# Kernel tuning notes

Measured on AMD Instinct MI355X. Metric: run time of the kernel, lower is better.

## Reference

```python
import jax, jax.numpy as jnp
import numpy as np


def setup_inputs() -> dict:
    key = jax.random.key(0)
    ks = jax.random.split(key, 6)
    B = 65536
    x = jax.random.normal(ks[0], (B, 784), dtype=jnp.float32)
    conv_w = jax.random.normal(ks[1], (3, 3), dtype=jnp.float32)
    fc1_w = jax.random.normal(ks[2], (100, 676), dtype=jnp.float32) * (1.0 / np.sqrt(676))
    fc1_b = jax.random.normal(ks[3], (100,), dtype=jnp.float32) * 0.01
    fc2_w = jax.random.normal(ks[4], (10, 100), dtype=jnp.float32) * (1.0 / np.sqrt(100))
    fc2_b = jax.random.normal(ks[5], (10,), dtype=jnp.float32) * 0.01
    return {"x": x, "conv_w": conv_w, "fc1_w": fc1_w, "fc1_b": fc1_b, "fc2_w": fc2_w, "fc2_b": fc2_b}


def reference(x, conv_w, fc1_w, fc1_b, fc2_w, fc2_b):
    B = x.shape[0]
    img = x.reshape(B, 1, 28, 28)  # NCHW, single channel
    kern = conv_w.reshape(1, 1, 3, 3)  # OIHW
    # 'valid' cross-correlation, matching the slicing-based Convolve()
    conv = jax.lax.conv_general_dilated(
        img, kern, window_strides=(1, 1), padding='VALID',
        dimension_numbers=('NCHW', 'OIHW', 'NCHW'))  # [B,1,26,26]
    h = conv.reshape(B, 26 * 26)
    h = jax.nn.relu(h @ fc1_w.T + fc1_b)
    out = h @ fc2_w.T + fc2_b
    return out
```

## Files before the change

### kernel.cpp

```cpp
#include <hip/hip_runtime.h>


typedef short  s16x8 __attribute__((ext_vector_type(8)));
typedef float  f32x4 __attribute__((ext_vector_type(4)));

#define BM   16
#define CSTR 712
#define HSTR 132
#define NT   8
#define KC   22

__device__ __forceinline__ unsigned short f2bf(float f) {
    unsigned int u = __builtin_bit_cast(unsigned int, f);
    u = (u + 0x7fffu + ((u >> 16) & 1u)) >> 16;
    return (unsigned short)u;
}

extern "C" __global__ void __launch_bounds__(256)
prep_w1(const float* __restrict__ W1, const float* __restrict__ b1,
        unsigned short* __restrict__ bw)
{
    int id = blockIdx.x * 256 + threadIdx.x;
    if (id >= NT * KC * 64) return;
    int lane = id & 63;
    int kc   = (id >> 6) % KC;
    int t    = id / (KC * 64);
    int n    = t * 16 + (lane & 15);
    int k0   = kc * 32 + (lane >> 4) * 8;
    unsigned short v[8];
#pragma unroll
    for (int j = 0; j < 8; ++j) {
        int k = k0 + j;
        float f = 0.f;
        if (n < 100) {
            if (k < 676)       f = W1[(size_t)n * 676 + k];
            else if (k == 676) f = b1[n];
        }
        v[j] = f2bf(f);
    }
    *(uint4*)(bw + (size_t)id * 8) = *(const uint4*)v;
}

extern "C" __global__ void __launch_bounds__(256, 6)
digit_model_fused(const float* __restrict__ x,
                  const float* __restrict__ cw9,
                  const unsigned short* __restrict__ bw,
                  const float* __restrict__ W2,
                  const float* __restrict__ b2,
                  float* __restrict__ out)
{
    __shared__ __align__(16) unsigned char smem[BM * CSTR * 2];
    unsigned short* cbuf = (unsigned short*)smem;
    float*          hbuf = (float*)smem;

    const int tid  = threadIdx.x;
    const int lane = tid & 63;
    const int wv   = tid >> 6;
    const int q    = lane >> 4;
    const int mn   = lane & 15;
    const int m0   = blockIdx.x * BM;

    float cw[9];
#pragma unroll
    for (int i = 0; i < 9; ++i) cw[i] = cw9[i];

    for (int p = tid; p < BM * 18; p += 256) {
        int mi = p / 18, qq = p - mi * 18;
        *(unsigned int*)(cbuf + mi * CSTR + 676 + qq * 2) = (qq == 0) ? 0x3F80u : 0u;
    }

    for (int task = tid; task < BM * 52; task += 256) {
        int mi = task / 52, rh = task - mi * 52, r = rh >> 1, h = rh & 1;
        const float* ip = x + (size_t)(m0 + mi) * 784 + r * 28 + h * 12;
        float acc[13];
#pragma unroll
        for (int c = 0; c < 13; ++c) acc[c] = 0.f;
#pragma unroll
        for (int dr = 0; dr < 3; ++dr) {
            float rowv[16];
            const float4* rp = (const float4*)(ip + dr * 28);
#pragma unroll
            for (int g = 0; g < 4; ++g) {
                float4 v = rp[g];
                rowv[g*4+0] = v.x; rowv[g*4+1] = v.y;
                rowv[g*4+2] = v.z; rowv[g*4+3] = v.w;
            }
#pragma unroll
            for (int dc = 0; dc < 3; ++dc) {
                float w = cw[dr*3+dc];
#pragma unroll
                for (int c = 0; c < 13; ++c)
                    acc[c] = fmaf(rowv[c + dc + h], w, acc[c]);
            }
        }
        unsigned short* dst = cbuf + mi * CSTR + r * 26 + h * 13;
        if (h == 0) {
#pragma unroll
            for (int c = 0; c < 12; c += 2)
                *(unsigned int*)(dst + c) =
                    (unsigned int)f2bf(acc[c]) | ((unsigned int)f2bf(acc[c+1]) << 16);
            dst[12] = f2bf(acc[12]);
        } else {
            dst[0] = f2bf(acc[0]);
#pragma unroll
            for (int c = 1; c < 13; c += 2)
                *(unsigned int*)(dst + c) =
                    (unsigned int)f2bf(acc[c]) | ((unsigned int)f2bf(acc[c+1]) << 16);
        }
    }
    __syncthreads();

    f32x4 acc0, acc1;
#pragma unroll
    for (int i = 0; i < 4; ++i) { acc0[i] = 0.f; acc1[i] = 0.f; }

    const unsigned short* arow = cbuf + mn * CSTR + q * 8;
    const uint4* bwv = (const uint4*)bw;
    const int t0 = wv, t1 = wv + 4;

    uint4 a  = *(const uint4*)(arow);
    uint4 b0 = bwv[(t0 * KC) * 64 + lane];
    uint4 b1 = bwv[(t1 * KC) * 64 + lane];
    for (int kc = 0; kc < KC; ++kc) {
        int kn = (kc + 1 < KC) ? kc + 1 : kc;
        uint4 na  = *(const uint4*)(arow + kn * 32);
        uint4 nb0 = bwv[(t0 * KC + kn) * 64 + lane];
        uint4 nb1 = bwv[(t1 * KC + kn) * 64 + lane];
        acc0 = __builtin_amdgcn_mfma_f32_16x16x32_bf16(
                   __builtin_bit_cast(s16x8, a), __builtin_bit_cast(s16x8, b0),
                   acc0, 0, 0, 0);
        acc1 = __builtin_amdgcn_mfma_f32_16x16x32_bf16(
                   __builtin_bit_cast(s16x8, a), __builtin_bit_cast(s16x8, b1),
                   acc1, 0, 0, 0);
        a = na; b0 = nb0; b1 = nb1;
    }
    __syncthreads();

#pragma unroll
    for (int r = 0; r < 4; ++r) {
        int row = q * 4 + r;
        float v0 = acc0[r]; v0 = v0 > 0.f ? v0 : 0.f;
        float v1 = acc1[r]; v1 = v1 > 0.f ? v1 : 0.f;
        hbuf[row * HSTR + t0 * 16 + mn] = v0;
        hbuf[row * HSTR + t1 * 16 + mn] = v1;
    }
    __syncthreads();

    for (int p = tid; p < BM * 10; p += 256) {
        int mi = p / 10, o = p - mi * 10;
        const float4* hv = (const float4*)(hbuf + mi * HSTR);
        const float4* w2 = (const float4*)(W2 + (size_t)o * 100);
        float s = b2[o];
#pragma unroll
        for (int g = 0; g < 25; ++g) {
            float4 h4 = hv[g], w4 = w2[g];
            s += h4.x*w4.x + h4.y*w4.y + h4.z*w4.z + h4.w*w4.w;
        }
        out[(size_t)(m0 + mi) * 10 + o] = s;
    }
}

extern "C" void kernel_launch(void* const* d_in, const int* in_sizes, int n_in,
                              void* d_out, int out_size, void* d_ws, size_t ws_size,
                              hipStream_t stream) {
    const float* x  = (const float*)d_in[0];
    const float* cw = (const float*)d_in[1];
    const float* W1 = (const float*)d_in[2];
    const float* b1 = (const float*)d_in[3];
    const float* W2 = (const float*)d_in[4];
    const float* b2 = (const float*)d_in[5];
    float* out = (float*)d_out;
    unsigned short* bw = (unsigned short*)d_ws;

    const int B = in_sizes[0] / 784;

    hipLaunchKernelGGL(prep_w1, dim3((NT * KC * 64 + 255) / 256), dim3(256),
                       0, stream, W1, b1, bw);
    hipLaunchKernelGGL(digit_model_fused, dim3(B / BM), dim3(256), 0, stream,
                       x, cw, bw, W2, b2, out);
}
```

Baseline: 327.8 us.

## Double row tile to 32 and reuse each W1 fragment across two MFMA row blocks

Raises the rows per block from 16 to 32 so each loaded W1 fragment feeds two MFMA row tiles. This halves the global W1 traffic per output row. The conv stage now gives each thread a full 26-wide output row instead of half a row, cutting redundant input loads. In exchange, LDS per block doubles, the occupancy hint drops from 6 to 4, register pressure rises, and the grid has half as many blocks.

```diff
diff --git a/kernel.cpp b/kernel.cpp
--- a/kernel.cpp
+++ b/kernel.cpp
@@ -4,7 +4,7 @@
 typedef short  s16x8 __attribute__((ext_vector_type(8)));
 typedef float  f32x4 __attribute__((ext_vector_type(4)));
 
-#define BM   16
+#define BM   32
 #define CSTR 712
 #define HSTR 132
 #define NT   8
@@ -41,7 +41,7 @@
     *(uint4*)(bw + (size_t)id * 8) = *(const uint4*)v;
 }
 
-extern "C" __global__ void __launch_bounds__(256, 6)
+extern "C" __global__ void __launch_bounds__(256, 4)
 digit_model_fused(const float* __restrict__ x,
                   const float* __restrict__ cw9,
                   const unsigned short* __restrict__ bw,
@@ -69,18 +69,18 @@
         *(unsigned int*)(cbuf + mi * CSTR + 676 + qq * 2) = (qq == 0) ? 0x3F80u : 0u;
     }
 
-    for (int task = tid; task < BM * 52; task += 256) {
-        int mi = task / 52, rh = task - mi * 52, r = rh >> 1, h = rh & 1;
-        const float* ip = x + (size_t)(m0 + mi) * 784 + r * 28 + h * 12;
-        float acc[13];
+    for (int task = tid; task < BM * 26; task += 256) {
+        int mi = task / 26, r = task - mi * 26;
+        const float* ip = x + (size_t)(m0 + mi) * 784 + r * 28;
+        float acc[26];
 #pragma unroll
-        for (int c = 0; c < 13; ++c) acc[c] = 0.f;
+        for (int c = 0; c < 26; ++c) acc[c] = 0.f;
 #pragma unroll
         for (int dr = 0; dr < 3; ++dr) {
-            float rowv[16];
+            float rowv[28];
             const float4* rp = (const float4*)(ip + dr * 28);
 #pragma unroll
-            for (int g = 0; g < 4; ++g) {
+            for (int g = 0; g < 7; ++g) {
                 float4 v = rp[g];
                 rowv[g*4+0] = v.x; rowv[g*4+1] = v.y;
                 rowv[g*4+2] = v.z; rowv[g*4+3] = v.w;
@@ -89,60 +89,55 @@
             for (int dc = 0; dc < 3; ++dc) {
                 float w = cw[dr*3+dc];
 #pragma unroll
-                for (int c = 0; c < 13; ++c)
-                    acc[c] = fmaf(rowv[c + dc + h], w, acc[c]);
+                for (int c = 0; c < 26; ++c)
+                    acc[c] = fmaf(rowv[c + dc], w, acc[c]);
             }
         }
-        unsigned short* dst = cbuf + mi * CSTR + r * 26 + h * 13;
-        if (h == 0) {
+        unsigned short* dst = cbuf + mi * CSTR + r * 26;
 #pragma unroll
-            for (int c = 0; c < 12; c += 2)
-                *(unsigned int*)(dst + c) =
-                    (unsigned int)f2bf(acc[c]) | ((unsigned int)f2bf(acc[c+1]) << 16);
-            dst[12] = f2bf(acc[12]);
-        } else {
-            dst[0] = f2bf(acc[0]);
-#pragma unroll
-            for (int c = 1; c < 13; c += 2)
-                *(unsigned int*)(dst + c) =
-                    (unsigned int)f2bf(acc[c]) | ((unsigned int)f2bf(acc[c+1]) << 16);
-        }
+        for (int c = 0; c < 26; c += 2)
+            *(unsigned int*)(dst + c) =
+                (unsigned int)f2bf(acc[c]) | ((unsigned int)f2bf(acc[c+1]) << 16);
     }
     __syncthreads();
 
-    f32x4 acc0, acc1;
+    f32x4 acc00, acc01, acc10, acc11;
 #pragma unroll
-    for (int i = 0; i < 4; ++i) { acc0[i] = 0.f; acc1[i] = 0.f; }
+    for (int i = 0; i < 4; ++i) { acc00[i]=0.f; acc01[i]=0.f; acc10[i]=0.f; acc11[i]=0.f; }
 
-    const unsigned short* arow = cbuf + mn * CSTR + q * 8;
+    const unsigned short* arow0 = cbuf + mn * CSTR + q * 8;
+    const unsigned short* arow1 = cbuf + (16 + mn) * CSTR + q * 8;
     const uint4* bwv = (const uint4*)bw;
     const int t0 = wv, t1 = wv + 4;
 
-    uint4 a  = *(const uint4*)(arow);
+    uint4 a0 = *(const uint4*)(arow0);
+    uint4 a1 = *(const uint4*)(arow1);
     uint4 b0 = bwv[(t0 * KC) * 64 + lane];
     uint4 b1 = bwv[(t1 * KC) * 64 + lane];
     for (int kc = 0; kc < KC; ++kc) {
         int kn = (kc + 1 < KC) ? kc + 1 : kc;
-        uint4 na  = *(const uint4*)(arow + kn * 32);
+        uint4 na0 = *(const uint4*)(arow0 + kn * 32);
+        uint4 na1 = *(const uint4*)(arow1 + kn * 32);
         uint4 nb0 = bwv[(t0 * KC + kn) * 64 + lane];
         uint4 nb1 = bwv[(t1 * KC + kn) * 64 + lane];
-        acc0 = __builtin_amdgcn_mfma_f32_16x16x32_bf16(
-                   __builtin_bit_cast(s16x8, a), __builtin_bit_cast(s16x8, b0),
-                   acc0, 0, 0, 0);
-        acc1 = __builtin_amdgcn_mfma_f32_16x16x32_bf16(
-                   __builtin_bit_cast(s16x8, a), __builtin_bit_cast(s16x8, b1),
-                   acc1, 0, 0, 0);
-        a = na; b0 = nb0; b1 = nb1;
+        s16x8 av0 = __builtin_bit_cast(s16x8, a0), av1 = __builtin_bit_cast(s16x8, a1);
+        s16x8 bv0 = __builtin_bit_cast(s16x8, b0), bv1 = __builtin_bit_cast(s16x8, b1);
+        acc00 = __builtin_amdgcn_mfma_f32_16x16x32_bf16(av0, bv0, acc00, 0, 0, 0);
+        acc01 = __builtin_amdgcn_mfma_f32_16x16x32_bf16(av0, bv1, acc01, 0, 0, 0);
+        acc10 = __builtin_amdgcn_mfma_f32_16x16x32_bf16(av1, bv0, acc10, 0, 0, 0);
+        acc11 = __builtin_amdgcn_mfma_f32_16x16x32_bf16(av1, bv1, acc11, 0, 0, 0);
+        a0 = na0; a1 = na1; b0 = nb0; b1 = nb1;
     }
     __syncthreads();
 
 #pragma unroll
     for (int r = 0; r < 4; ++r) {
         int row = q * 4 + r;
-        float v0 = acc0[r]; v0 = v0 > 0.f ? v0 : 0.f;
-        float v1 = acc1[r]; v1 = v1 > 0.f ? v1 : 0.f;
-        hbuf[row * HSTR + t0 * 16 + mn] = v0;
-        hbuf[row * HSTR + t1 * 16 + mn] = v1;
+        float v;
+        v = acc00[r]; v = v > 0.f ? v : 0.f; hbuf[ row       * HSTR + t0 * 16 + mn] = v;
+        v = acc01[r]; v = v > 0.f ? v : 0.f; hbuf[ row       * HSTR + t1 * 16 + mn] = v;
+        v = acc10[r]; v = v > 0.f ? v : 0.f; hbuf[(row + 16) * HSTR + t0 * 16 + mn] = v;
+        v = acc11[r]; v = v > 0.f ? v : 0.f; hbuf[(row + 16) * HSTR + t1 * 16 + mn] = v;
     }
     __syncthreads();
 
```

Result: no change. 332.9 us (+1.5%).

## Stage input tile in LDS as bf16 with coalesced loads before convolution

Applied to the files above, without the earlier changes.

Each block now loads its 16 input images from global memory with fully coalesced float4 reads, converts them to bf16 and stores them in a new LDS buffer. The 3x3 convolution then reads rows from LDS and computes a full 26-wide output row per task, instead of overlapping half-row gathers from global memory. This targets redundant and poorly coalesced global reads of x, which is the dominant traffic. In exchange the kernel uses more LDS (occupancy hint lowered from 6 to 4) and quantizes the input to bf16 before the convolution, which adds rounding error.

```diff
diff --git a/kernel.cpp b/kernel.cpp
--- a/kernel.cpp
+++ b/kernel.cpp
@@ -5,6 +5,7 @@
 typedef float  f32x4 __attribute__((ext_vector_type(4)));
 
 #define BM   16
+#define XSTR 788
 #define CSTR 712
 #define HSTR 132
 #define NT   8
@@ -14,6 +15,12 @@
     unsigned int u = __builtin_bit_cast(unsigned int, f);
     u = (u + 0x7fffu + ((u >> 16) & 1u)) >> 16;
     return (unsigned short)u;
+}
+__device__ __forceinline__ float bflo(unsigned int u) {
+    return __builtin_bit_cast(float, u << 16);
+}
+__device__ __forceinline__ float bfhi(unsigned int u) {
+    return __builtin_bit_cast(float, u & 0xffff0000u);
 }
 
 extern "C" __global__ void __launch_bounds__(256)
@@ -41,7 +48,7 @@
     *(uint4*)(bw + (size_t)id * 8) = *(const uint4*)v;
 }
 
-extern "C" __global__ void __launch_bounds__(256, 6)
+extern "C" __global__ void __launch_bounds__(256, 4)
 digit_model_fused(const float* __restrict__ x,
                   const float* __restrict__ cw9,
                   const unsigned short* __restrict__ bw,
@@ -49,8 +56,9 @@
                   const float* __restrict__ b2,
                   float* __restrict__ out)
 {
-    __shared__ __align__(16) unsigned char smem[BM * CSTR * 2];
-    unsigned short* cbuf = (unsigned short*)smem;
+    __shared__ __align__(16) unsigned char smem[BM * XSTR * 2 + BM * CSTR * 2];
+    unsigned short* xbuf = (unsigned short*)smem;
+    unsigned short* cbuf = (unsigned short*)(smem + BM * XSTR * 2);
     float*          hbuf = (float*)smem;
 
     const int tid  = threadIdx.x;
@@ -69,44 +77,48 @@
         *(unsigned int*)(cbuf + mi * CSTR + 676 + qq * 2) = (qq == 0) ? 0x3F80u : 0u;
     }
 
-    for (int task = tid; task < BM * 52; task += 256) {
-        int mi = task / 52, rh = task - mi * 52, r = rh >> 1, h = rh & 1;
-        const float* ip = x + (size_t)(m0 + mi) * 784 + r * 28 + h * 12;
-        float acc[13];
+    {
+        const float4* xg = (const float4*)(x + (size_t)m0 * 784);
+        for (int p = tid; p < BM * 196; p += 256) {
+            int mi = p / 196, g = p - mi * 196;
+            float4 v = xg[p];
+            unsigned int lo = (unsigned int)f2bf(v.x) | ((unsigned int)f2bf(v.y) << 16);
+            unsigned int hi = (unsigned int)f2bf(v.z) | ((unsigned int)f2bf(v.w) << 16);
+            uint2 w; w.x = lo; w.y = hi;
+            *(uint2*)(xbuf + mi * XSTR + g * 4) = w;
+        }
+    }
+    __syncthreads();
+
+    for (int task = tid; task < BM * 26; task += 256) {
+        int mi = task / 26, r = task - mi * 26;
+        const unsigned short* irow = xbuf + mi * XSTR + r * 28;
+        float acc[26];
 #pragma unroll
-        for (int c = 0; c < 13; ++c) acc[c] = 0.f;
+        for (int c = 0; c < 26; ++c) acc[c] = 0.f;
 #pragma unroll
         for (int dr = 0; dr < 3; ++dr) {
-            float rowv[16];
-            const float4* rp = (const float4*)(ip + dr * 28);
+            float rowv[28];
+            const uint2* rp = (const uint2*)(irow + dr * 28);
 #pragma unroll
-            for (int g = 0; g < 4; ++g) {
-                float4 v = rp[g];
-                rowv[g*4+0] = v.x; rowv[g*4+1] = v.y;
-                rowv[g*4+2] = v.z; rowv[g*4+3] = v.w;
+            for (int g = 0; g < 7; ++g) {
+                uint2 u = rp[g];
+                rowv[g*4+0] = bflo(u.x); rowv[g*4+1] = bfhi(u.x);
+                rowv[g*4+2] = bflo(u.y); rowv[g*4+3] = bfhi(u.y);
             }
 #pragma unroll
             for (int dc = 0; dc < 3; ++dc) {
                 float w = cw[dr*3+dc];
 #pragma unroll
-                for (int c = 0; c < 13; ++c)
-                    acc[c] = fmaf(rowv[c + dc + h], w, acc[c]);
+                for (int c = 0; c < 26; ++c)
+                    acc[c] = fmaf(rowv[c + dc], w, acc[c]);
             }
         }
-        unsigned short* dst = cbuf + mi * CSTR + r * 26 + h * 13;
-        if (h == 0) {
+        unsigned short* dst = cbuf + mi * CSTR + r * 26;
 #pragma unroll
-            for (int c = 0; c < 12; c += 2)
-                *(unsigned int*)(dst + c) =
-                    (unsigned int)f2bf(acc[c]) | ((unsigned int)f2bf(acc[c+1]) << 16);
-            dst[12] = f2bf(acc[12]);
-        } else {
-            dst[0] = f2bf(acc[0]);
-#pragma unroll
-            for (int c = 1; c < 13; c += 2)
-                *(unsigned int*)(dst + c) =
-                    (unsigned int)f2bf(acc[c]) | ((unsigned int)f2bf(acc[c+1]) << 16);
-        }
+        for (int c = 0; c < 26; c += 2)
+            *(unsigned int*)(dst + c) =
+                (unsigned int)f2bf(acc[c]) | ((unsigned int)f2bf(acc[c+1]) << 16);
     }
     __syncthreads();
 
```

Result: slower. 364.9 us (+11.3%).
